# Performance work log

Hardware: AMD Instinct MI355X
Metric: run time of the kernel (lower is better)

## Reference

```python
import jax, jax.numpy as jnp
import numpy as np


def setup_inputs() -> dict:
    key = jax.random.key(0)
    k1, k2 = jax.random.split(key)
    x = jax.random.normal(k1, (32, 64, 64, 64), dtype=jnp.float32)  # [B, C, H, W]
    limit = 3 ** 0.5
    embeddings = jax.random.uniform(k2, (64, 512), dtype=jnp.float32,
                                    minval=-limit, maxval=limit)  # [D, K]
    return {"x": x, "embeddings": embeddings}


def reference(x, embeddings):
    B, D, H, W = x.shape
    # NCHW -> NHWC -> [N, D]
    flat_x = jnp.transpose(x, (0, 2, 3, 1)).reshape(-1, D)
    distances = (
        jnp.sum(flat_x ** 2, axis=1, keepdims=True)
        - 2.0 * flat_x @ embeddings
        + jnp.sum(embeddings ** 2, axis=0, keepdims=True)
    )
    encoding_indices = jnp.argmin(distances, axis=1)  # [N]
    # gather codebook rows: embeddings.T is [K, D]
    quantized = embeddings.T[encoding_indices].reshape(B, H, W, D)
    quantized = jnp.transpose(quantized, (0, 3, 1, 2))  # back to NCHW
    commitment_loss = jnp.mean((x - jax.lax.stop_gradient(quantized)) ** 2)
    # straight-through estimator
    quantized_ste = x + jax.lax.stop_gradient(quantized - x)
    return quantized_ste, commitment_loss, encoding_indices.reshape(B, -1)
```

## Files before the change

kernel.cpp:

```cpp
#include <hip/hip_runtime.h>

#define D      64
#define K      512
#define Q_OFF  0
#define L_OFF  8388608
#define I_OFF  8388609

#define WS_ET    0
#define WS_EN    32768
#define WS_ENH   33280
#define WS_PART  33792

#define B_LO_OFF 4096

#define SEL_SCALE 16384.0f
#define SEL_BIAS  (160.0f * 16384.0f)

typedef __attribute__((ext_vector_type(8))) short short8;
typedef __attribute__((ext_vector_type(4))) float f32x4;

static __device__ __forceinline__ unsigned short f2bf(float f) {
    unsigned u = __float_as_uint(f);
    u += 0x7fffu + ((u >> 16) & 1u);
    return (unsigned short)(u >> 16);
}
static __device__ __forceinline__ float bf2f(unsigned short h) {
    return __uint_as_float(((unsigned)h) << 16);
}

__device__ __forceinline__ void gload_lds16(const float* g, float* l) {
    __builtin_amdgcn_global_load_lds(
        (const __attribute__((address_space(1))) unsigned int*)g,
        (__attribute__((address_space(3))) unsigned int*)l, 16, 0, 0);
}

__global__ __launch_bounds__(256) void vq_prep(const float* __restrict__ E,
                                               float* __restrict__ ws,
                                               float* __restrict__ out) {
    int g = blockIdx.x * 256 + threadIdx.x;
    int t = g >> 6, lane = g & 63;
    int col = lane & 15, kg = lane >> 4;
    int code = t * 16 + col;
    short8* bhp = (short8*)out;
    short8* blp = (short8*)out + B_LO_OFF;
#pragma unroll
    for (int s = 0; s < 2; ++s) {
        short8 h, l;
#pragma unroll
        for (int j = 0; j < 8; ++j) {
            int k = s * 32 + kg * 8 + j;
            float v = -E[k * K + code];
            unsigned short hb = f2bf(v);
            h[j] = (short)hb;
            l[j] = (short)f2bf(v - bf2f(hb));
        }
        bhp[(t * 2 + s) * 64 + lane] = h;
        blp[(t * 2 + s) * 64 + lane] = l;
    }
    if (g < K) {
        float nsq = 0.f;
#pragma unroll 8
        for (int d = 0; d < D; ++d) {
            float v = E[d * K + g];
            ws[WS_ET + g * D + d] = v;
            nsq = fmaf(v, v, nsq);
        }
        ws[WS_EN + g]  = nsq;
        ws[WS_ENH + g] = 0.5f * nsq;
    }
}

__global__ __launch_bounds__(128, 4) void vq_dist(const float* __restrict__ x,
                                                  const float* __restrict__ ws,
                                                  float* __restrict__ out) {
    __shared__ float sbuf[3][1024];
    __shared__ float senh[512];

    const int tid = threadIdx.x, w = tid >> 6, lane = tid & 63;
    const int col = lane & 15, rowg = lane >> 4;
    const int pixw = blockIdx.x * 64 + w * 32;

    const float* bh  = (const float*)out;
    const float* bl  = (const float*)out + B_LO_OFF * 4;

    {
#pragma unroll
        for (int q = 0; q < 1; ++q) gload_lds16(ws + WS_ENH + tid * 4, senh + tid * 4);
        gload_lds16(bh + tid * 4,       sbuf[0] + tid * 4);
        gload_lds16(bl + tid * 4,       sbuf[0] + 512 + tid * 4);
        gload_lds16(bh + 512 + tid * 4, sbuf[1] + tid * 4);
        gload_lds16(bl + 512 + tid * 4, sbuf[1] + 512 + tid * 4);
    }

    short8 ah[2][2], al[2][2];
#pragma unroll
    for (int mt = 0; mt < 2; ++mt) {
        int pix = pixw + mt * 16 + col;
        const float* xp = x + ((size_t)(pix >> 12) << 18) + (pix & 4095);
#pragma unroll
        for (int s = 0; s < 2; ++s) {
            short8 h, l;
#pragma unroll
            for (int j = 0; j < 8; ++j) {
                float v = xp[(size_t)(s * 32 + rowg * 8 + j) << 12];
                unsigned short hb = f2bf(v);
                h[j] = (short)hb;
                l[j] = (short)f2bf(v - bf2f(hb));
            }
            ah[mt][s] = h; al[mt][s] = l;
        }
    }

    unsigned m1[2][4], m2[2][4];
#pragma unroll
    for (int mt = 0; mt < 2; ++mt)
#pragma unroll
        for (int r = 0; r < 4; ++r) { m1[mt][r] = 0xFFFFFFFFu; m2[mt][r] = 0xFFFFFFFFu; }

    int cbuf = 0;
    for (int c = 0; c < 32; ++c) {
        asm volatile("s_waitcnt vmcnt(2)" ::: "memory");
        __builtin_amdgcn_s_barrier();
        __builtin_amdgcn_sched_barrier(0);

        if (c + 2 < 32) {
            int sb2 = (cbuf >= 1) ? cbuf - 1 : 2;
            const float* sh = bh + (c + 2) * 512;
            const float* sl = bl + (c + 2) * 512;
            gload_lds16(sh + tid * 4, sbuf[sb2] + tid * 4);
            gload_lds16(sl + tid * 4, sbuf[sb2] + 512 + tid * 4);
        }

        const short8* sb = (const short8*)sbuf[cbuf];
        const float ev = senh[c * 16 + col];
        const unsigned codev = (unsigned)(c * 16 + col);

        short8 cbh0 = sb[lane];
        short8 cbh1 = sb[64 + lane];
        short8 cbl0 = sb[128 + lane];
        short8 cbl1 = sb[192 + lane];

        f32x4 acc0 = { ev, ev, ev, ev };
        f32x4 acc1 = { ev, ev, ev, ev };
        __builtin_amdgcn_s_setprio(1);
        acc0 = __builtin_amdgcn_mfma_f32_16x16x32_bf16(ah[0][0], cbh0, acc0, 0, 0, 0);
        acc1 = __builtin_amdgcn_mfma_f32_16x16x32_bf16(ah[1][0], cbh0, acc1, 0, 0, 0);
        acc0 = __builtin_amdgcn_mfma_f32_16x16x32_bf16(al[0][0], cbh0, acc0, 0, 0, 0);
        acc1 = __builtin_amdgcn_mfma_f32_16x16x32_bf16(al[1][0], cbh0, acc1, 0, 0, 0);
        acc0 = __builtin_amdgcn_mfma_f32_16x16x32_bf16(ah[0][0], cbl0, acc0, 0, 0, 0);
        acc1 = __builtin_amdgcn_mfma_f32_16x16x32_bf16(ah[1][0], cbl0, acc1, 0, 0, 0);
        acc0 = __builtin_amdgcn_mfma_f32_16x16x32_bf16(ah[0][1], cbh1, acc0, 0, 0, 0);
        acc1 = __builtin_amdgcn_mfma_f32_16x16x32_bf16(ah[1][1], cbh1, acc1, 0, 0, 0);
        acc0 = __builtin_amdgcn_mfma_f32_16x16x32_bf16(al[0][1], cbh1, acc0, 0, 0, 0);
        acc1 = __builtin_amdgcn_mfma_f32_16x16x32_bf16(al[1][1], cbh1, acc1, 0, 0, 0);
        acc0 = __builtin_amdgcn_mfma_f32_16x16x32_bf16(ah[0][1], cbl1, acc0, 0, 0, 0);
        acc1 = __builtin_amdgcn_mfma_f32_16x16x32_bf16(ah[1][1], cbl1, acc1, 0, 0, 0);
        __builtin_amdgcn_s_setprio(0);

#pragma unroll
        for (int r = 0; r < 4; ++r) {
            unsigned p0 = (((unsigned)fmaf(acc0[r], SEL_SCALE, SEL_BIAS)) << 9) + codev;
            m2[0][r] = min(m2[0][r], max(m1[0][r], p0));
            m1[0][r] = min(m1[0][r], p0);
            unsigned p1 = (((unsigned)fmaf(acc1[r], SEL_SCALE, SEL_BIAS)) << 9) + codev;
            m2[1][r] = min(m2[1][r], max(m1[1][r], p1));
            m1[1][r] = min(m1[1][r], p1);
        }

        cbuf = (cbuf == 2) ? 0 : cbuf + 1;
    }

    unsigned* outu = (unsigned*)out;
#pragma unroll
    for (int mt = 0; mt < 2; ++mt)
#pragma unroll
        for (int r = 0; r < 4; ++r) {
            unsigned v1 = m1[mt][r], v2 = m2[mt][r];
#pragma unroll
            for (int m = 1; m < 16; m <<= 1) {
                unsigned o1 = (unsigned)__shfl_xor((int)v1, m, 16);
                unsigned o2 = (unsigned)__shfl_xor((int)v2, m, 16);
                v2 = min(max(v1, o1), min(v2, o2));
                v1 = min(v1, o1);
            }
            if (col == r) {
                int p = pixw + mt * 16 + rowg * 4 + r;
                unsigned c1 = v1 & 511u, c2 = v2 & 511u;
                outu[I_OFF + p] = c1 | (c2 << 16);
            }
        }
}

__device__ __forceinline__ float dot32(const float* __restrict__ er,
                                       const float* __restrict__ xv) {
    const float4* e4 = (const float4*)er;
    float a0 = 0.f, a1 = 0.f, a2 = 0.f, a3 = 0.f;
#pragma unroll
    for (int q = 0; q < 8; ++q) {
        float4 e = e4[q];
        a0 = fmaf(xv[4*q+0], e.x, a0);
        a1 = fmaf(xv[4*q+1], e.y, a1);
        a2 = fmaf(xv[4*q+2], e.z, a2);
        a3 = fmaf(xv[4*q+3], e.w, a3);
    }
    return (a0 + a1) + (a2 + a3);
}

__global__ __launch_bounds__(256) void vq_out(const float* __restrict__ x,
                                              const float* __restrict__ ws,
                                              float* __restrict__ out,
                                              float* __restrict__ partial) {
    const float* ET = ws + WS_ET;
    const float* EN = ws + WS_EN;
    const int tid  = threadIdx.x;
    const int pl   = tid & 127;
    const int half = tid >> 7;
    const int n    = blockIdx.x * 128 + pl;
    const int b    = n >> 12;
    const int hw   = n & 4095;

    const float* xp = x + ((size_t)b << 18) + ((size_t)half << 17) + hw;
    float xv[32];
#pragma unroll
    for (int d = 0; d < 32; ++d) xv[d] = xp[(size_t)d << 12];

    unsigned packed = ((const unsigned*)out)[I_OFF + n];
    int c1 = (int)(packed & 0xffffu), c2 = (int)(packed >> 16);

    float dp1 = dot32(ET + (c1 << 6) + half * 32, xv);
    float dp2 = dot32(ET + (c2 << 6) + half * 32, xv);

    __shared__ float2 sdot[2][128];
    sdot[half][pl] = make_float2(dp1, dp2);
    __syncthreads();
    float2 lo = sdot[0][pl], hi = sdot[1][pl];
    float d1 = fmaf(-2.f, lo.x + hi.x, EN[c1]);
    float d2 = fmaf(-2.f, lo.y + hi.y, EN[c2]);
    bool sw = (d2 < d1) || (d2 == d1 && c2 < c1);
    int bestk = sw ? c2 : c1;

    if (!half) out[I_OFF + n] = (float)bestk;

    const float* qv = ET + (bestk << 6) + half * 32;
    float* op = out + Q_OFF + ((size_t)b << 18) + ((size_t)half << 17) + hw;
    float lsum = 0.f;
#pragma unroll
    for (int d = 0; d < 32; ++d) {
        float qd = qv[d];
        op[(size_t)d << 12] = qd;
        float diff = xv[d] - qd;
        lsum = fmaf(diff, diff, lsum);
    }

#pragma unroll
    for (int off = 32; off > 0; off >>= 1)
        lsum += __shfl_down(lsum, off, 64);
    __shared__ float wsum[4];
    if ((tid & 63) == 0) wsum[tid >> 6] = lsum;
    __syncthreads();
    if (tid == 0)
        partial[blockIdx.x] = (wsum[0] + wsum[1]) + (wsum[2] + wsum[3]);
}

__global__ __launch_bounds__(256) void vq_final(const float* __restrict__ partial,
                                                float* __restrict__ out) {
    int t = threadIdx.x;
    float s = ((partial[t] + partial[t + 256]) + partial[t + 512]) + partial[t + 768];
#pragma unroll
    for (int off = 32; off > 0; off >>= 1)
        s += __shfl_down(s, off, 64);
    __shared__ float wsum[4];
    if ((t & 63) == 0) wsum[t >> 6] = s;
    __syncthreads();
    if (t == 0)
        out[L_OFF] = ((wsum[0] + wsum[1]) + (wsum[2] + wsum[3])) * (1.f / 8388608.f);
}

extern "C" void kernel_launch(void* const* d_in, const int* in_sizes, int n_in,
                              void* d_out, int out_size, void* d_ws, size_t ws_size,
                              hipStream_t stream) {
    const float* x = (const float*)d_in[0];
    const float* E = (const float*)d_in[1];
    float* out = (float*)d_out;
    float* ws  = (float*)d_ws;

    hipLaunchKernelGGL(vq_prep,  dim3(8),    dim3(256), 0, stream, E, ws, out);
    hipLaunchKernelGGL(vq_dist,  dim3(2048), dim3(128), 0, stream, x, ws, out);
    hipLaunchKernelGGL(vq_out,   dim3(1024), dim3(256), 0, stream, x, ws, out, ws + WS_PART);
    hipLaunchKernelGGL(vq_final, dim3(1),    dim3(256), 0, stream, ws + WS_PART, out);
}
```

Baseline: 69.45 us.

## Fuse distance argmin and output/loss kernels into one kernel

Merges the MFMA distance/top-2 selection kernel with the refinement, quantized-output and loss kernel. Candidate indices now pass through shared memory instead of a global round trip, and the separate launch goes away. The bf16 split codebooks move from the output buffer to the workspace, and the final reduction now sums 2048 partials. In exchange, the per-block tail work runs inside a 128-thread block with launch bounds (128,4), and x is re-read for the epilogue.

```diff
diff --git a/kernel.cpp b/kernel.cpp
--- a/kernel.cpp
+++ b/kernel.cpp
@@ -10,8 +10,8 @@
 #define WS_EN    32768
 #define WS_ENH   33280
 #define WS_PART  33792
-
-#define B_LO_OFF 4096
+#define WS_BH    36864
+#define WS_BL    53248
 
 #define SEL_SCALE 16384.0f
 #define SEL_BIAS  (160.0f * 16384.0f)
@@ -35,14 +35,13 @@
 }
 
 __global__ __launch_bounds__(256) void vq_prep(const float* __restrict__ E,
-                                               float* __restrict__ ws,
-                                               float* __restrict__ out) {
+                                               float* __restrict__ ws) {
     int g = blockIdx.x * 256 + threadIdx.x;
     int t = g >> 6, lane = g & 63;
     int col = lane & 15, kg = lane >> 4;
     int code = t * 16 + col;
-    short8* bhp = (short8*)out;
-    short8* blp = (short8*)out + B_LO_OFF;
+    short8* bhp = (short8*)(ws + WS_BH);
+    short8* blp = (short8*)(ws + WS_BL);
 #pragma unroll
     for (int s = 0; s < 2; ++s) {
         short8 h, l;
@@ -70,27 +69,42 @@
     }
 }
 
-__global__ __launch_bounds__(128, 4) void vq_dist(const float* __restrict__ x,
-                                                  const float* __restrict__ ws,
-                                                  float* __restrict__ out) {
+__device__ __forceinline__ float dot32(const float* __restrict__ er,
+                                       const float* __restrict__ xv) {
+    const float4* e4 = (const float4*)er;
+    float a0 = 0.f, a1 = 0.f, a2 = 0.f, a3 = 0.f;
+#pragma unroll
+    for (int q = 0; q < 8; ++q) {
+        float4 e = e4[q];
+        a0 = fmaf(xv[4*q+0], e.x, a0);
+        a1 = fmaf(xv[4*q+1], e.y, a1);
+        a2 = fmaf(xv[4*q+2], e.z, a2);
+        a3 = fmaf(xv[4*q+3], e.w, a3);
+    }
+    return (a0 + a1) + (a2 + a3);
+}
+
+__global__ __launch_bounds__(128, 4) void vq_fused(const float* __restrict__ x,
+                                                   float* __restrict__ ws,
+                                                   float* __restrict__ out,
+                                                   float* __restrict__ partial) {
     __shared__ float sbuf[3][1024];
     __shared__ float senh[512];
+    __shared__ unsigned sc[64];
+    __shared__ float2 sdot[2][64];
 
     const int tid = threadIdx.x, w = tid >> 6, lane = tid & 63;
     const int col = lane & 15, rowg = lane >> 4;
     const int pixw = blockIdx.x * 64 + w * 32;
 
-    const float* bh  = (const float*)out;
-    const float* bl  = (const float*)out + B_LO_OFF * 4;
-
-    {
-#pragma unroll
-        for (int q = 0; q < 1; ++q) gload_lds16(ws + WS_ENH + tid * 4, senh + tid * 4);
-        gload_lds16(bh + tid * 4,       sbuf[0] + tid * 4);
-        gload_lds16(bl + tid * 4,       sbuf[0] + 512 + tid * 4);
-        gload_lds16(bh + 512 + tid * 4, sbuf[1] + tid * 4);
-        gload_lds16(bl + 512 + tid * 4, sbuf[1] + 512 + tid * 4);
-    }
+    const float* bh = ws + WS_BH;
+    const float* bl = ws + WS_BL;
+
+    gload_lds16(ws + WS_ENH + tid * 4, senh + tid * 4);
+    gload_lds16(bh + tid * 4,       sbuf[0] + tid * 4);
+    gload_lds16(bl + tid * 4,       sbuf[0] + 512 + tid * 4);
+    gload_lds16(bh + 512 + tid * 4, sbuf[1] + tid * 4);
+    gload_lds16(bl + 512 + tid * 4, sbuf[1] + 512 + tid * 4);
 
     short8 ah[2][2], al[2][2];
 #pragma unroll
@@ -119,7 +133,8 @@
 
     int cbuf = 0;
     for (int c = 0; c < 32; ++c) {
-        asm volatile("s_waitcnt vmcnt(2)" ::: "memory");
+        if (c < 31) asm volatile("s_waitcnt vmcnt(2)" ::: "memory");
+        else        asm volatile("s_waitcnt vmcnt(0)" ::: "memory");
         __builtin_amdgcn_s_barrier();
         __builtin_amdgcn_sched_barrier(0);
 
@@ -170,7 +185,6 @@
         cbuf = (cbuf == 2) ? 0 : cbuf + 1;
     }
 
-    unsigned* outu = (unsigned*)out;
 #pragma unroll
     for (int mt = 0; mt < 2; ++mt)
 #pragma unroll
@@ -183,54 +197,29 @@
                 v2 = min(max(v1, o1), min(v2, o2));
                 v1 = min(v1, o1);
             }
-            if (col == r) {
-                int p = pixw + mt * 16 + rowg * 4 + r;
-                unsigned c1 = v1 & 511u, c2 = v2 & 511u;
-                outu[I_OFF + p] = c1 | (c2 << 16);
-            }
-        }
-}
-
-__device__ __forceinline__ float dot32(const float* __restrict__ er,
-                                       const float* __restrict__ xv) {
-    const float4* e4 = (const float4*)er;
-    float a0 = 0.f, a1 = 0.f, a2 = 0.f, a3 = 0.f;
-#pragma unroll
-    for (int q = 0; q < 8; ++q) {
-        float4 e = e4[q];
-        a0 = fmaf(xv[4*q+0], e.x, a0);
-        a1 = fmaf(xv[4*q+1], e.y, a1);
-        a2 = fmaf(xv[4*q+2], e.z, a2);
-        a3 = fmaf(xv[4*q+3], e.w, a3);
-    }
-    return (a0 + a1) + (a2 + a3);
-}
-
-__global__ __launch_bounds__(256) void vq_out(const float* __restrict__ x,
-                                              const float* __restrict__ ws,
-                                              float* __restrict__ out,
-                                              float* __restrict__ partial) {
+            if (col == r)
+                sc[w * 32 + mt * 16 + rowg * 4 + r] = (v1 & 511u) | ((v2 & 511u) << 16);
+        }
+    __syncthreads();
+
     const float* ET = ws + WS_ET;
     const float* EN = ws + WS_EN;
-    const int tid  = threadIdx.x;
-    const int pl   = tid & 127;
-    const int half = tid >> 7;
-    const int n    = blockIdx.x * 128 + pl;
+    const int pl   = tid & 63;
+    const int half = tid >> 6;
+    const int n    = blockIdx.x * 64 + pl;
     const int b    = n >> 12;
     const int hw   = n & 4095;
 
-    const float* xp = x + ((size_t)b << 18) + ((size_t)half << 17) + hw;
-    float xv[32];
-#pragma unroll
-    for (int d = 0; d < 32; ++d) xv[d] = xp[(size_t)d << 12];
-
-    unsigned packed = ((const unsigned*)out)[I_OFF + n];
-    int c1 = (int)(packed & 0xffffu), c2 = (int)(packed >> 16);
-
-    float dp1 = dot32(ET + (c1 << 6) + half * 32, xv);
-    float dp2 = dot32(ET + (c2 << 6) + half * 32, xv);
-
-    __shared__ float2 sdot[2][128];
+    unsigned pk = sc[pl];
+    int c1 = (int)(pk & 0xffffu), c2 = (int)(pk >> 16);
+
+    const float* xp2 = x + ((size_t)b << 18) + ((size_t)half << 17) + hw;
+    float xv2[32];
+#pragma unroll
+    for (int d = 0; d < 32; ++d) xv2[d] = xp2[(size_t)d << 12];
+
+    float dp1 = dot32(ET + (c1 << 6) + half * 32, xv2);
+    float dp2 = dot32(ET + (c2 << 6) + half * 32, xv2);
     sdot[half][pl] = make_float2(dp1, dp2);
     __syncthreads();
     float2 lo = sdot[0][pl], hi = sdot[1][pl];
@@ -248,24 +237,26 @@
     for (int d = 0; d < 32; ++d) {
         float qd = qv[d];
         op[(size_t)d << 12] = qd;
-        float diff = xv[d] - qd;
+        float diff = xv2[d] - qd;
         lsum = fmaf(diff, diff, lsum);
     }
 
 #pragma unroll
     for (int off = 32; off > 0; off >>= 1)
         lsum += __shfl_down(lsum, off, 64);
-    __shared__ float wsum[4];
+    __shared__ float wsum[2];
     if ((tid & 63) == 0) wsum[tid >> 6] = lsum;
     __syncthreads();
     if (tid == 0)
-        partial[blockIdx.x] = (wsum[0] + wsum[1]) + (wsum[2] + wsum[3]);
+        partial[blockIdx.x] = wsum[0] + wsum[1];
 }
 
 __global__ __launch_bounds__(256) void vq_final(const float* __restrict__ partial,
                                                 float* __restrict__ out) {
     int t = threadIdx.x;
-    float s = ((partial[t] + partial[t + 256]) + partial[t + 512]) + partial[t + 768];
+    float s = 0.f;
+#pragma unroll
+    for (int i = 0; i < 8; ++i) s += partial[t + 256 * i];
 #pragma unroll
     for (int off = 32; off > 0; off >>= 1)
         s += __shfl_down(s, off, 64);
@@ -284,8 +275,7 @@
     float* out = (float*)d_out;
     float* ws  = (float*)d_ws;
 
-    hipLaunchKernelGGL(vq_prep,  dim3(8),    dim3(256), 0, stream, E, ws, out);
-    hipLaunchKernelGGL(vq_dist,  dim3(2048), dim3(128), 0, stream, x, ws, out);
-    hipLaunchKernelGGL(vq_out,   dim3(1024), dim3(256), 0, stream, x, ws, out, ws + WS_PART);
+    hipLaunchKernelGGL(vq_prep,  dim3(8),    dim3(256), 0, stream, E, ws);
+    hipLaunchKernelGGL(vq_fused, dim3(2048), dim3(128), 0, stream, x, ws, out, ws + WS_PART);
     hipLaunchKernelGGL(vq_final, dim3(1),    dim3(256), 0, stream, ws + WS_PART, out);
 }
```

New measurement: 62.15 us. 10.5% less time.
